# Kernel tuning notes

Hardware: AMD Instinct MI355X
Metric: run time of the kernel (lower is better)

## Reference

```python
import jax
import jax.numpy as jnp
import numpy as np
from jax import lax

STD = 1.0          # prior gaussian std
LAMBDA_2 = 0.1
LAMBDA_3 = 1000.0
MAX_ITER = 20
TOL = 1e-05
DIM = 512
SEQ = 4096


def mahalanobis_dist(P, Q, M):
    # dist[i,j] = (P_i - Q_j)^T M (P_i - Q_j)
    pMp = jnp.einsum('id,de,ie->i', P, M, P)          # [m]
    qMq = jnp.einsum('jd,de,je->j', Q, M, Q)          # [n]
    cross = P @ (M + M.T) @ Q.T                        # [m,n]
    return pMp[:, None] + qMq[None, :] - cross


def sinkhorn_iterative(K, alpha, beta, max_iter=MAX_ITER, tol=TOL):
    # Faithful replication of the torch loop (check at iter%20==1 or iter==max_iter).
    ainvK = K / alpha
    KT = K.T

    def check(u, v, it):
        v2 = beta / (KT @ u)
        u2 = 1.0 / (ainvK @ v2)
        crit = jnp.max(jnp.abs(jnp.sum(jnp.abs(v2 * (KT @ u2) - beta), axis=0)))  # inf-norm
        return u2, v2, it + 1, jnp.abs(crit) < tol

    def cond(state):
        _, _, it, done = state
        return (it < max_iter) & (~done)

    def body(state):
        u, v, it, done = state
        u = 1.0 / (ainvK @ (beta / (KT @ u)))
        it = it + 1
        do_check = ((it % 20) == 1) | (it == max_iter)
        return lax.cond(do_check,
                        lambda: check(u, v, it),
                        lambda: (u, v, it, done))

    u0 = alpha
    v0 = jnp.zeros_like(beta)
    u, v, _, _ = lax.while_loop(cond, body,
                                (u0, v0, jnp.asarray(0, jnp.int32), jnp.asarray(False)))
    return u, v


def W_M(P, Q, M):
    m, n = P.shape[0], Q.shape[0]
    dtype = P.dtype
    dist = mahalanobis_dist(P, Q, M)                                  # [m,n]
    alpha = (jnp.arange(1, m + 1, dtype=dtype) / m)[:, None]          # [m,1]
    beta = (jnp.arange(1, n + 1, dtype=dtype) / n)[:, None]           # [n,1]
    rel = alpha - beta.T                                              # [m,n]
    denom = jnp.sqrt(1.0 / n**2 + 1.0 / m**2)
    prior = (1.0 / (STD * np.sqrt(2.0 * np.pi))) * jnp.exp(
        -(jnp.abs(rel) / denom) ** 2 / (2.0 * STD**2))
    K = prior * jnp.exp(-(dist - LAMBDA_2 / (rel**2 + 1.0)) / LAMBDA_3)
    Kng = lax.stop_gradient(K)                                        # torch computed K under no_grad
    u, v = sinkhorn_iterative(Kng, alpha, beta)
    F = lax.stop_gradient(u * Kng * v.T)                              # detached transport plan
    return jnp.sum(F * dist)


def setup_inputs() -> dict:
    key = jax.random.key(0)
    kP, kQ, kR, kS, kM = jax.random.split(key, 5)
    P = jax.random.normal(kP, (SEQ, DIM), dtype=jnp.float32)
    Q = jax.random.normal(kQ, (SEQ, DIM), dtype=jnp.float32)
    R = jax.random.normal(kR, (SEQ, DIM), dtype=jnp.float32)
    S = jax.random.normal(kS, (SEQ, DIM), dtype=jnp.float32)
    M = jax.random.normal(kM, (DIM, DIM), dtype=jnp.float32)          # learned metric parameter
    return {"P": P, "Q": Q, "R": R, "S": S, "M": M}


def reference(P, Q, R, S, M):
    return W_M(P, Q, M) - W_M(R, S, M)
```

## Files before the change

### kernel.cpp

```cpp
#include <hip/hip_runtime.h>
#include <hip/hip_bf16.h>
#include <math.h>

#define SEQ   4096
#define DIM   512
#define BW    24
#define NDIAG 49
#define TW    56
#define VSTR  4608
#define VOFF  256
#define INV_N (1.0f/4096.0f)

#define OFF_KT   0
#define SZ_T     (2*SEQ*TW)
#define OFF_KC   (OFF_KT + SZ_T)
#define OFF_DT   (OFF_KC + SZ_T)
#define OFF_VEC  (OFF_DT + SZ_T)
#define SZ_VEC   (6*VSTR)
#define OFF_PX   (OFF_VEC + SZ_VEC)
#define SZ_PX    (4*SEQ)
#define OFF_SC   (OFF_PX + SZ_PX)
#define SZ_SC    16
#define OFF_BBF  (OFF_SC + SZ_SC)
#define SZ_BBF   (DIM*DIM/2)
#define OFF_XBF  (OFF_BBF + SZ_BBF)
#define SZ_XBF   (4*SEQ*DIM/2)
#define OFF_GBF  (OFF_XBF + SZ_XBF)
#define SZ_GBF   (2*SEQ*DIM/2)
#define WS_FLOATS (OFF_GBF + SZ_GBF)

typedef __attribute__((ext_vector_type(8))) short short8;
typedef __attribute__((ext_vector_type(4))) float f32x4;

__device__ __forceinline__ ushort f2bfh(float f) {
    __hip_bfloat16 h = __float2bfloat16(f);
    return *reinterpret_cast<ushort*>(&h);
}
__device__ __forceinline__ float bf2f(ushort u) {
    union { unsigned u; float f; } w; w.u = ((unsigned)u) << 16; return w.f;
}

__device__ __forceinline__ void gload16(void* lds, const void* g) {
    __builtin_amdgcn_global_load_lds(
        (const __attribute__((address_space(1))) unsigned int*)g,
        (__attribute__((address_space(3))) unsigned int*)lds,
        16, 0, 0);
}

#define ZQUADS (OFF_BBF/4)
#define ZBLK   ((ZQUADS + 255)/256)
#define BBLK   1024
#define CBLK   8192
#define PREP_BLOCKS (ZBLK + BBLK + CBLK)

__global__ void kprep(const float* __restrict__ P, const float* __restrict__ Q,
                      const float* __restrict__ R, const float* __restrict__ S,
                      const float* __restrict__ M, float* __restrict__ ws) {
    int b = blockIdx.x, tid = threadIdx.x;
    if (b < ZBLK) {
        int q = b*256 + tid;
        if (q < ZQUADS)
            *reinterpret_cast<float4*>(&ws[(size_t)q*4]) = (float4){0.f,0.f,0.f,0.f};
    } else if (b < ZBLK + BBLK) {
        int idx = (b - ZBLK)*256 + tid;
        int d = idx >> 9, e = idx & 511;
        ((ushort*)(ws + OFF_BBF))[idx] = f2bfh(M[d*DIM + e] + M[e*DIM + d]);
    } else {
        int cb = b - (ZBLK + BBLK);
        int z = cb >> 11;
        const float* src = (z==0) ? P : (z==1) ? Q : (z==2) ? R : S;
        size_t idx = ((size_t)(cb & 2047)*256 + tid)*4;
        float4 v = *reinterpret_cast<const float4*>(&src[idx]);
        ushort4 o;
        o.x = f2bfh(v.x); o.y = f2bfh(v.y); o.z = f2bfh(v.z); o.w = f2bfh(v.w);
        *reinterpret_cast<ushort4*>(((ushort*)(ws + OFF_XBF)) + (size_t)z*SEQ*DIM + idx) = o;
    }
}

__launch_bounds__(256, 4)
__global__ void kgemm5(const ushort* __restrict__ Xbf, const ushort* __restrict__ Bbf,
                       ushort* __restrict__ GBbf, float* __restrict__ pX) {
    int z = blockIdx.z;
    const ushort* Xh = Xbf + (size_t)z*SEQ*DIM;
    int i0 = blockIdx.x * 128;
    int j0 = blockIdx.y * 128;
    __shared__ ushort As[2*4096];
    __shared__ ushort Bs[2*4096];
    int tid = threadIdx.x, wv = tid >> 6, l = tid & 63;
    int h = l >> 4, lr = l & 15;
    int wrow = (wv >> 1)*64, wcol = (wv & 1)*64;

    auto stageA = [&](int buf, int kc) {
        #pragma unroll
        for (int s2 = 0; s2 < 2; ++s2) {
            int seg = wv*2 + s2;
            gload16((char*)As + (size_t)buf*8192 + seg*1024,
                    &Xh[(size_t)(i0 + (seg&1)*64 + l)*DIM + kc + (seg>>1)*8]);
        }
    };
    auto stageB = [&](int buf, int kc) {
        #pragma unroll
        for (int s2 = 0; s2 < 2; ++s2) {
            int seg = wv*2 + s2;
            int col = seg*16 + (l >> 2);
            int cs = (l & 3) ^ (col & 3);
            gload16((char*)Bs + (size_t)buf*8192 + seg*1024,
                    &Bbf[(size_t)(j0+col)*DIM + kc + cs*8]);
        }
    };

    f32x4 acc[4][4];
    #pragma unroll
    for (int a = 0; a < 4; ++a)
        #pragma unroll
        for (int b = 0; b < 4; ++b) acc[a][b] = (f32x4){0.f,0.f,0.f,0.f};

    stageA(0, 0); stageB(0, 0);
    __syncthreads();
    for (int t = 0; t < 16; ++t) {
        int cur = t & 1;
        if (t < 15) { stageA(cur ^ 1, (t+1)*32); stageB(cur ^ 1, (t+1)*32); }
        short8 a8[4], b8[4];
        #pragma unroll
        for (int rt = 0; rt < 4; ++rt) {
            int row = wrow + rt*16 + lr;
            a8[rt] = *reinterpret_cast<const short8*>(
                (const char*)As + (size_t)cur*8192 + h*2048 + row*16);
        }
        #pragma unroll
        for (int ct = 0; ct < 4; ++ct) {
            int col = wcol + ct*16 + lr;
            int c = h ^ (col & 3);
            b8[ct] = *reinterpret_cast<const short8*>(
                (const char*)Bs + (size_t)cur*8192 + col*64 + c*16);
        }
        #pragma unroll
        for (int rt = 0; rt < 4; ++rt)
            #pragma unroll
            for (int ct = 0; ct < 4; ++ct)
                acc[rt][ct] = __builtin_amdgcn_mfma_f32_16x16x32_bf16(a8[rt], b8[ct], acc[rt][ct], 0, 0, 0);
        __syncthreads();
    }

    #pragma unroll
    for (int rt = 0; rt < 4; ++rt) {
        #pragma unroll
        for (int r = 0; r < 4; ++r) {
            int row = wrow + rt*16 + h*4 + r;
            float v = 0.f;
            #pragma unroll
            for (int ct = 0; ct < 4; ++ct) {
                int col = wcol + ct*16 + lr;
                float cv = acc[rt][ct][r];
                float xv = bf2f(Xh[(size_t)(i0+row)*DIM + j0 + col]);
                v = fmaf(cv, xv, v);
                if ((z & 1) == 0)
                    GBbf[((size_t)((z>>1)*SEQ + i0 + row))*DIM + j0 + col] = f2bfh(cv);
            }
            v += __shfl_xor(v, 1); v += __shfl_xor(v, 2);
            v += __shfl_xor(v, 4); v += __shfl_xor(v, 8);
            if (lr == 0) atomicAdd(&pX[(size_t)z*SEQ + i0 + row], 0.5f*v);
        }
    }
}

__launch_bounds__(64)
__global__ void kband3(const ushort* __restrict__ GBbf, const ushort* __restrict__ Xbf,
                       const float* __restrict__ pX,
                       float* __restrict__ Ktb, float* __restrict__ Kcb,
                       float* __restrict__ Dt) {
    int g = blockIdx.y;
    int i0 = blockIdx.x * 16;
    int l = threadIdx.x;
    const ushort* A = GBbf + (size_t)g*SEQ*DIM;
    const ushort* Y = Xbf + (size_t)(1 + 2*g)*SEQ*DIM;
    const float* pM = pX + (size_t)(2*g)*SEQ;
    const float* qM = pX + (size_t)(2*g+1)*SEQ;
    int jbase = i0 - BW;
    int arow = i0 + (l & 15);
    int koff = (l >> 4) * 8;
    int jcl[4];
    #pragma unroll
    for (int ct = 0; ct < 4; ++ct) {
        int j = jbase + ct*16 + (l & 15);
        jcl[ct] = min(max(j, 0), SEQ-1);
    }
    f32x4 acc[4];
    #pragma unroll
    for (int ct = 0; ct < 4; ++ct) acc[ct] = (f32x4){0.f,0.f,0.f,0.f};
    #pragma unroll
    for (int ks = 0; ks < 16; ++ks) {
        int kk = ks*32 + koff;
        short8 af = *reinterpret_cast<const short8*>(&A[(size_t)arow*DIM + kk]);
        #pragma unroll
        for (int ct = 0; ct < 4; ++ct) {
            short8 bf = *reinterpret_cast<const short8*>(&Y[(size_t)jcl[ct]*DIM + kk]);
            acc[ct] = __builtin_amdgcn_mfma_f32_16x16x32_bf16(af, bf, acc[ct], 0, 0, 0);
        }
    }
    #pragma unroll
    for (int ct = 0; ct < 4; ++ct) {
        #pragma unroll
        for (int r = 0; r < 4; ++r) {
            int i = i0 + (l >> 4)*4 + r;
            int j = jbase + ct*16 + (l & 15);
            int d = j - i;
            if (d >= -BW && d <= BW && j >= 0 && j < SEQ) {
                float dist = pM[i] + qM[j] - acc[ct][r];
                float fd = (float)d;
                float rel = fd * (1.0f/4096.0f);
                float cd = -0.91893853f - 0.25f*fd*fd + 1e-4f/(rel*rel + 1.0f);
                float Kv = expf(cd - dist*1e-3f);
                Ktb[((size_t)g*SEQ + i)*TW + (d + BW)] = Kv;
                Kcb[((size_t)g*SEQ + j)*TW + (BW - d)] = Kv;
                Dt [((size_t)g*SEQ + i)*TW + (d + BW)] = dist;
            }
        }
    }
}

#define SR3  32
#define SB3  384
__launch_bounds__(256)
__global__ void ksink3(const float* __restrict__ Ktb, const float* __restrict__ Kcb,
                       float* __restrict__ vecs, float* __restrict__ sc,
                       int nsteps, int firstT, int alphaInit,
                       int vstep, int ustep, int cstep, int gated, int inSlot, int outSlot) {
    int g = blockIdx.y;
    if (gated && sc[g] < 1e-5f) return;
    int r0 = blockIdx.x * SR3;
    int ext = 24 * nsteps;
    __shared__ float bufA[SB3];
    __shared__ float bufB[SB3];
    __shared__ float vsave[SB3];
    __shared__ float red[256];
    float* bin = bufA;
    float* bout = bufB;
    int base = r0 - ext;
    int range0 = SR3 + 2*ext;
    const float* vin = vecs + (size_t)(inSlot*2 + g)*VSTR;
    for (int L = threadIdx.x; L < SB3; L += 256) {
        int gr = base + L;
        float v = 0.f;
        if (L < range0 && gr >= 0 && gr < SEQ)
            v = alphaInit ? (gr+1)*INV_N : vin[VOFF + gr];
        bufA[L] = v;
        bufB[L] = 0.f;
    }
    __syncthreads();
    float critloc = 0.f;
    for (int m = 0; m < nsteps; ++m) {
        int e = 24*(nsteps - 1 - m);
        int lo = ext - e;
        int cnt = SR3 + 2*e;
        int typeT = firstT ^ (m & 1);
        const float* tap0 = (typeT ? Kcb : Ktb) + (size_t)g*SEQ*TW;
        for (int t = threadIdx.x; t < cnt; t += 256) {
            int L = lo + t;
            int gr = base + L;
            float o = 0.f;
            if (gr >= 0 && gr < SEQ) {
                const float* tap = tap0 + (size_t)gr*TW;
                float s = 0.f;
                #pragma unroll
                for (int c = 0; c < 14; ++c) {
                    float4 k4 = *reinterpret_cast<const float4*>(tap + c*4);
                    s = fmaf(k4.x, bin[L + c*4 + 0 - BW], s);
                    s = fmaf(k4.y, bin[L + c*4 + 1 - BW], s);
                    s = fmaf(k4.z, bin[L + c*4 + 2 - BW], s);
                    s = fmaf(k4.w, bin[L + c*4 + 3 - BW], s);
                }
                float ab = (gr+1)*INV_N;
                o = ab * __builtin_amdgcn_rcpf(s);
                if (m == vstep) {
                    vecs[(size_t)(4 + g)*VSTR + VOFF + gr] = o;
                    if (cstep >= 0) vsave[L] = o;
                }
                if (m == ustep)
                    vecs[(size_t)g*VSTR + VOFF + gr] = o;
                if (m == cstep)
                    critloc += fabsf(vsave[L]*s - ab);
            }
            bout[L] = o;
        }
        __syncthreads();
        float* tmp = bin; bin = bout; bout = tmp;
    }
    if (threadIdx.x < SR3) {
        int gr = r0 + threadIdx.x;
        vecs[(size_t)(outSlot*2 + g)*VSTR + VOFF + gr] = bin[ext + threadIdx.x];
    }
    if (cstep >= 0) {
        red[threadIdx.x] = critloc;
        __syncthreads();
        for (int s = 128; s > 0; s >>= 1) {
            if (threadIdx.x < s) red[threadIdx.x] += red[threadIdx.x + s];
            __syncthreads();
        }
        if (threadIdx.x == 0) atomicAdd(&sc[g], red[0]);
    }
}

__launch_bounds__(256)
__global__ void kfinal(const float* __restrict__ Ktb, const float* __restrict__ Dt,
                       const float* __restrict__ vecs, float* __restrict__ sc) {
    int g = blockIdx.y;
    int i = blockIdx.x * 256 + threadIdx.x;
    const float* kt = Ktb + ((size_t)g*SEQ + i)*TW;
    const float* dt = Dt  + ((size_t)g*SEQ + i)*TW;
    const float* u = vecs + (size_t)g*VSTR + VOFF;
    const float* v = vecs + (size_t)(4 + g)*VSTR + VOFF;
    float ss = 0.f;
    #pragma unroll
    for (int c = 0; c < 14; ++c) {
        float4 k4 = *reinterpret_cast<const float4*>(kt + c*4);
        float4 d4 = *reinterpret_cast<const float4*>(dt + c*4);
        ss += k4.x * d4.x * v[i + c*4 + 0 - BW];
        ss += k4.y * d4.y * v[i + c*4 + 1 - BW];
        ss += k4.z * d4.z * v[i + c*4 + 2 - BW];
        ss += k4.w * d4.w * v[i + c*4 + 3 - BW];
    }
    ss *= u[i];
    __shared__ float red[256];
    red[threadIdx.x] = ss;
    __syncthreads();
    for (int s = 128; s > 0; s >>= 1) {
        if (threadIdx.x < s) red[threadIdx.x] += red[threadIdx.x + s];
        __syncthreads();
    }
    if (threadIdx.x == 0) atomicAdd(&sc[2+g], red[0]);
}

__global__ void kout(const float* __restrict__ sc, float* __restrict__ out) {
    out[0] = sc[2] - sc[3];
}

extern "C" void kernel_launch(void* const* d_in, const int* in_sizes, int n_in,
                              void* d_out, int out_size, void* d_ws, size_t ws_size,
                              hipStream_t stream) {
    const float* P = (const float*)d_in[0];
    const float* Q = (const float*)d_in[1];
    const float* R = (const float*)d_in[2];
    const float* S = (const float*)d_in[3];
    const float* M = (const float*)d_in[4];
    float* ws = (float*)d_ws;
    if (ws_size < (size_t)WS_FLOATS * sizeof(float)) return;

    float*  Ktb = ws + OFF_KT;
    float*  Kcb = ws + OFF_KC;
    float*  Dt  = ws + OFF_DT;
    float*  vec = ws + OFF_VEC;
    float*  pX  = ws + OFF_PX;
    float*  sc  = ws + OFF_SC;
    ushort* Bbf = (ushort*)(ws + OFF_BBF);
    ushort* Xbf = (ushort*)(ws + OFF_XBF);
    ushort* GBbf= (ushort*)(ws + OFF_GBF);

    kprep <<<dim3(PREP_BLOCKS), dim3(256), 0, stream>>>(P, Q, R, S, M, ws);
    kgemm5<<<dim3(32, 4, 4),    dim3(256), 0, stream>>>(Xbf, Bbf, GBbf, pX);
    kband3<<<dim3(256, 2),      dim3(64),  0, stream>>>(GBbf, Xbf, pX, Ktb, Kcb, Dt);

    ksink3<<<dim3(128,2), dim3(256), 0, stream>>>(Ktb, Kcb, vec, sc,  5, 1, 1,  2,  3,  4, 0, 0, 1);
    ksink3<<<dim3(128,2), dim3(256), 0, stream>>>(Ktb, Kcb, vec, sc,  6, 0, 0, -1, -1, -1, 1, 1, 1);
    ksink3<<<dim3(128,2), dim3(256), 0, stream>>>(Ktb, Kcb, vec, sc,  6, 0, 0, -1, -1, -1, 1, 1, 1);
    ksink3<<<dim3(128,2), dim3(256), 0, stream>>>(Ktb, Kcb, vec, sc,  6, 0, 0, -1, -1, -1, 1, 1, 1);
    ksink3<<<dim3(128,2), dim3(256), 0, stream>>>(Ktb, Kcb, vec, sc,  6, 0, 0, -1, -1, -1, 1, 1, 1);
    ksink3<<<dim3(128,2), dim3(256), 0, stream>>>(Ktb, Kcb, vec, sc,  6, 0, 0, -1, -1, -1, 1, 1, 1);
    ksink3<<<dim3(128,2), dim3(256), 0, stream>>>(Ktb, Kcb, vec, sc,  7, 0, 0,  5, -1, -1, 1, 1, 0);

    kfinal<<<dim3(16,2), dim3(256), 0, stream>>>(Ktb, Dt, vec, sc);
    kout  <<<dim3(1),    dim3(1),   0, stream>>>(sc, (float*)d_out);
}
```

Measured before the change: 160.3 us.

## Merge Sinkhorn launches, final reduction and output into one cooperative kernel

Replaces the seven ksink3 launches plus kfinal and kout with a single cooperative kernel that runs the same Sinkhorn super-steps separated by grid-wide syncs. The convergence gate becomes a per-block skip flag read after the first grid sync. The final transport-cost reduction is folded in, using 32 rows per block instead of 256-row blocks. This is meant to remove per-launch overhead and launch gaps, at the price of grid.sync costs and needing all 256 blocks to be co-resident.

```diff
diff --git a/kernel.cpp b/kernel.cpp
--- a/kernel.cpp
+++ b/kernel.cpp
@@ -1,6 +1,9 @@
 #include <hip/hip_runtime.h>
+#include <hip/hip_cooperative_groups.h>
 #include <hip/hip_bf16.h>
 #include <math.h>
+
+namespace cg = cooperative_groups;
 
 #define SEQ   4096
 #define DIM   512
@@ -221,118 +224,134 @@
 
 #define SR3  32
 #define SB3  384
-__launch_bounds__(256)
-__global__ void ksink3(const float* __restrict__ Ktb, const float* __restrict__ Kcb,
-                       float* __restrict__ vecs, float* __restrict__ sc,
-                       int nsteps, int firstT, int alphaInit,
-                       int vstep, int ustep, int cstep, int gated, int inSlot, int outSlot) {
+#define NSS  7
+__launch_bounds__(256, 4)
+__global__ void ksinkcoop(const float* __restrict__ Ktb, const float* __restrict__ Kcb,
+                          const float* __restrict__ Dt, float* __restrict__ vecs,
+                          float* __restrict__ sc, float* __restrict__ out) {
+    cg::grid_group grid = cg::this_grid();
+    const int NS[NSS] = {5,6,6,6,6,6,7};
+    const int FT[NSS] = {1,0,0,0,0,0,0};
+    const int AI[NSS] = {1,0,0,0,0,0,0};
+    const int VS[NSS] = {2,-1,-1,-1,-1,-1,5};
+    const int US[NSS] = {3,-1,-1,-1,-1,-1,-1};
+    const int CS[NSS] = {4,-1,-1,-1,-1,-1,-1};
+    const int IN[NSS] = {0,1,1,1,1,1,1};
+    const int OU[NSS] = {1,1,1,1,1,1,0};
     int g = blockIdx.y;
-    if (gated && sc[g] < 1e-5f) return;
     int r0 = blockIdx.x * SR3;
-    int ext = 24 * nsteps;
     __shared__ float bufA[SB3];
     __shared__ float bufB[SB3];
     __shared__ float vsave[SB3];
     __shared__ float red[256];
-    float* bin = bufA;
-    float* bout = bufB;
-    int base = r0 - ext;
-    int range0 = SR3 + 2*ext;
-    const float* vin = vecs + (size_t)(inSlot*2 + g)*VSTR;
-    for (int L = threadIdx.x; L < SB3; L += 256) {
-        int gr = base + L;
-        float v = 0.f;
-        if (L < range0 && gr >= 0 && gr < SEQ)
-            v = alphaInit ? (gr+1)*INV_N : vin[VOFF + gr];
-        bufA[L] = v;
-        bufB[L] = 0.f;
-    }
-    __syncthreads();
-    float critloc = 0.f;
-    for (int m = 0; m < nsteps; ++m) {
-        int e = 24*(nsteps - 1 - m);
-        int lo = ext - e;
-        int cnt = SR3 + 2*e;
-        int typeT = firstT ^ (m & 1);
-        const float* tap0 = (typeT ? Kcb : Ktb) + (size_t)g*SEQ*TW;
-        for (int t = threadIdx.x; t < cnt; t += 256) {
-            int L = lo + t;
-            int gr = base + L;
-            float o = 0.f;
-            if (gr >= 0 && gr < SEQ) {
-                const float* tap = tap0 + (size_t)gr*TW;
-                float s = 0.f;
-                #pragma unroll
-                for (int c = 0; c < 14; ++c) {
-                    float4 k4 = *reinterpret_cast<const float4*>(tap + c*4);
-                    s = fmaf(k4.x, bin[L + c*4 + 0 - BW], s);
-                    s = fmaf(k4.y, bin[L + c*4 + 1 - BW], s);
-                    s = fmaf(k4.z, bin[L + c*4 + 2 - BW], s);
-                    s = fmaf(k4.w, bin[L + c*4 + 3 - BW], s);
+    bool skip = false;
+
+    for (int ss = 0; ss < NSS; ++ss) {
+        if (!(ss > 0 && skip)) {
+            int nsteps = NS[ss];
+            int vstep = VS[ss], ustep = US[ss], cstep = CS[ss];
+            int ext = 24*nsteps;
+            int base = r0 - ext;
+            int range0 = SR3 + 2*ext;
+            const float* vin = vecs + (size_t)(IN[ss]*2 + g)*VSTR;
+            for (int L = threadIdx.x; L < SB3; L += 256) {
+                int gr = base + L;
+                float v = 0.f;
+                if (L < range0 && gr >= 0 && gr < SEQ)
+                    v = AI[ss] ? (gr+1)*INV_N : vin[VOFF + gr];
+                bufA[L] = v;
+                bufB[L] = 0.f;
+            }
+            __syncthreads();
+            float critloc = 0.f;
+            float* bin = bufA;
+            float* bout = bufB;
+            for (int m = 0; m < nsteps; ++m) {
+                int e = 24*(nsteps - 1 - m);
+                int lo = ext - e;
+                int cnt = SR3 + 2*e;
+                int typeT = FT[ss] ^ (m & 1);
+                const float* tap0 = (typeT ? Kcb : Ktb) + (size_t)g*SEQ*TW;
+                for (int t = threadIdx.x; t < cnt; t += 256) {
+                    int L = lo + t;
+                    int gr = base + L;
+                    float o = 0.f;
+                    if (gr >= 0 && gr < SEQ) {
+                        const float* tap = tap0 + (size_t)gr*TW;
+                        float s = 0.f;
+                        #pragma unroll
+                        for (int c = 0; c < 14; ++c) {
+                            float4 k4 = *reinterpret_cast<const float4*>(tap + c*4);
+                            s = fmaf(k4.x, bin[L + c*4 + 0 - BW], s);
+                            s = fmaf(k4.y, bin[L + c*4 + 1 - BW], s);
+                            s = fmaf(k4.z, bin[L + c*4 + 2 - BW], s);
+                            s = fmaf(k4.w, bin[L + c*4 + 3 - BW], s);
+                        }
+                        float ab = (gr+1)*INV_N;
+                        o = ab * __builtin_amdgcn_rcpf(s);
+                        if (m == vstep) {
+                            vecs[(size_t)(4 + g)*VSTR + VOFF + gr] = o;
+                            if (cstep >= 0) vsave[L] = o;
+                        }
+                        if (m == ustep)
+                            vecs[(size_t)g*VSTR + VOFF + gr] = o;
+                        if (m == cstep)
+                            critloc += fabsf(vsave[L]*s - ab);
+                    }
+                    bout[L] = o;
                 }
-                float ab = (gr+1)*INV_N;
-                o = ab * __builtin_amdgcn_rcpf(s);
-                if (m == vstep) {
-                    vecs[(size_t)(4 + g)*VSTR + VOFF + gr] = o;
-                    if (cstep >= 0) vsave[L] = o;
+                __syncthreads();
+                float* tmp = bin; bin = bout; bout = tmp;
+            }
+            if (threadIdx.x < SR3) {
+                int gr = r0 + threadIdx.x;
+                vecs[(size_t)(OU[ss]*2 + g)*VSTR + VOFF + gr] = bin[ext + threadIdx.x];
+            }
+            if (cstep >= 0) {
+                red[threadIdx.x] = critloc;
+                __syncthreads();
+                for (int s2 = 128; s2 > 0; s2 >>= 1) {
+                    if (threadIdx.x < s2) red[threadIdx.x] += red[threadIdx.x + s2];
+                    __syncthreads();
                 }
-                if (m == ustep)
-                    vecs[(size_t)g*VSTR + VOFF + gr] = o;
-                if (m == cstep)
-                    critloc += fabsf(vsave[L]*s - ab);
-            }
-            bout[L] = o;
-        }
+                if (threadIdx.x == 0) atomicAdd(&sc[g], red[0]);
+            }
+        }
+        grid.sync();
+        if (ss == 0) skip = (sc[g] < 1e-5f);
+    }
+
+    {
+        float partial = 0.f;
+        if (threadIdx.x < SR3) {
+            int i = r0 + threadIdx.x;
+            const float* kt = Ktb + ((size_t)g*SEQ + i)*TW;
+            const float* dt = Dt  + ((size_t)g*SEQ + i)*TW;
+            const float* u = vecs + (size_t)g*VSTR + VOFF;
+            const float* v = vecs + (size_t)(4 + g)*VSTR + VOFF;
+            float ssum = 0.f;
+            #pragma unroll
+            for (int c = 0; c < 14; ++c) {
+                float4 k4 = *reinterpret_cast<const float4*>(kt + c*4);
+                float4 d4 = *reinterpret_cast<const float4*>(dt + c*4);
+                ssum += k4.x * d4.x * v[i + c*4 + 0 - BW];
+                ssum += k4.y * d4.y * v[i + c*4 + 1 - BW];
+                ssum += k4.z * d4.z * v[i + c*4 + 2 - BW];
+                ssum += k4.w * d4.w * v[i + c*4 + 3 - BW];
+            }
+            partial = ssum * u[i];
+        }
+        red[threadIdx.x] = partial;
         __syncthreads();
-        float* tmp = bin; bin = bout; bout = tmp;
-    }
-    if (threadIdx.x < SR3) {
-        int gr = r0 + threadIdx.x;
-        vecs[(size_t)(outSlot*2 + g)*VSTR + VOFF + gr] = bin[ext + threadIdx.x];
-    }
-    if (cstep >= 0) {
-        red[threadIdx.x] = critloc;
-        __syncthreads();
-        for (int s = 128; s > 0; s >>= 1) {
-            if (threadIdx.x < s) red[threadIdx.x] += red[threadIdx.x + s];
+        for (int s2 = 128; s2 > 0; s2 >>= 1) {
+            if (threadIdx.x < s2) red[threadIdx.x] += red[threadIdx.x + s2];
             __syncthreads();
         }
-        if (threadIdx.x == 0) atomicAdd(&sc[g], red[0]);
-    }
-}
-
-__launch_bounds__(256)
-__global__ void kfinal(const float* __restrict__ Ktb, const float* __restrict__ Dt,
-                       const float* __restrict__ vecs, float* __restrict__ sc) {
-    int g = blockIdx.y;
-    int i = blockIdx.x * 256 + threadIdx.x;
-    const float* kt = Ktb + ((size_t)g*SEQ + i)*TW;
-    const float* dt = Dt  + ((size_t)g*SEQ + i)*TW;
-    const float* u = vecs + (size_t)g*VSTR + VOFF;
-    const float* v = vecs + (size_t)(4 + g)*VSTR + VOFF;
-    float ss = 0.f;
-    #pragma unroll
-    for (int c = 0; c < 14; ++c) {
-        float4 k4 = *reinterpret_cast<const float4*>(kt + c*4);
-        float4 d4 = *reinterpret_cast<const float4*>(dt + c*4);
-        ss += k4.x * d4.x * v[i + c*4 + 0 - BW];
-        ss += k4.y * d4.y * v[i + c*4 + 1 - BW];
-        ss += k4.z * d4.z * v[i + c*4 + 2 - BW];
-        ss += k4.w * d4.w * v[i + c*4 + 3 - BW];
-    }
-    ss *= u[i];
-    __shared__ float red[256];
-    red[threadIdx.x] = ss;
-    __syncthreads();
-    for (int s = 128; s > 0; s >>= 1) {
-        if (threadIdx.x < s) red[threadIdx.x] += red[threadIdx.x + s];
-        __syncthreads();
-    }
-    if (threadIdx.x == 0) atomicAdd(&sc[2+g], red[0]);
-}
-
-__global__ void kout(const float* __restrict__ sc, float* __restrict__ out) {
-    out[0] = sc[2] - sc[3];
+        if (threadIdx.x == 0) atomicAdd(&sc[2+g], red[0]);
+    }
+    grid.sync();
+    if (blockIdx.x == 0 && blockIdx.y == 0 && threadIdx.x == 0)
+        out[0] = sc[2] - sc[3];
 }
 
 extern "C" void kernel_launch(void* const* d_in, const int* in_sizes, int n_in,
@@ -360,14 +379,9 @@
     kgemm5<<<dim3(32, 4, 4),    dim3(256), 0, stream>>>(Xbf, Bbf, GBbf, pX);
     kband3<<<dim3(256, 2),      dim3(64),  0, stream>>>(GBbf, Xbf, pX, Ktb, Kcb, Dt);
 
-    ksink3<<<dim3(128,2), dim3(256), 0, stream>>>(Ktb, Kcb, vec, sc,  5, 1, 1,  2,  3,  4, 0, 0, 1);
-    ksink3<<<dim3(128,2), dim3(256), 0, stream>>>(Ktb, Kcb, vec, sc,  6, 0, 0, -1, -1, -1, 1, 1, 1);
-    ksink3<<<dim3(128,2), dim3(256), 0, stream>>>(Ktb, Kcb, vec, sc,  6, 0, 0, -1, -1, -1, 1, 1, 1);
-    ksink3<<<dim3(128,2), dim3(256), 0, stream>>>(Ktb, Kcb, vec, sc,  6, 0, 0, -1, -1, -1, 1, 1, 1);
-    ksink3<<<dim3(128,2), dim3(256), 0, stream>>>(Ktb, Kcb, vec, sc,  6, 0, 0, -1, -1, -1, 1, 1, 1);
-    ksink3<<<dim3(128,2), dim3(256), 0, stream>>>(Ktb, Kcb, vec, sc,  6, 0, 0, -1, -1, -1, 1, 1, 1);
-    ksink3<<<dim3(128,2), dim3(256), 0, stream>>>(Ktb, Kcb, vec, sc,  7, 0, 0,  5, -1, -1, 1, 1, 0);
-
-    kfinal<<<dim3(16,2), dim3(256), 0, stream>>>(Ktb, Dt, vec, sc);
-    kout  <<<dim3(1),    dim3(1),   0, stream>>>(sc, (float*)d_out);
-}
+    float* outp = (float*)d_out;
+    void* args[] = { (void*)&Ktb, (void*)&Kcb, (void*)&Dt,
+                     (void*)&vec, (void*)&sc, (void*)&outp };
+    hipLaunchCooperativeKernel((void*)ksinkcoop, dim3(128, 2), dim3(256),
+                               args, 0, stream);
+}
```

Measured after the change: 353.3 us. 120% more time.
